# Optimization experiments

Hardware: AMD Instinct MI355X
Metric: run time of the kernel (lower is better)

Reference implementation:

```python
import jax, jax.numpy as jnp
import numpy as np

EPS = 1e-7
B, F, C, H, W, D = 2, 2, 64, 32, 104, 96


def _pix_homog(h, w):
    ys, xs = jnp.meshgrid(jnp.arange(h, dtype=jnp.float32),
                          jnp.arange(w, dtype=jnp.float32), indexing='ij')
    return jnp.stack([xs.ravel(), ys.ravel(), jnp.ones(h * w, jnp.float32)], 0)  # [3, H*W]


def setup_inputs() -> dict:
    key = jax.random.key(0)
    k1, k2 = jax.random.split(key)
    current_feats = jax.random.normal(k1, (B, C, H, W), jnp.float32)
    lookup_feats = jax.random.normal(k2, (B, F, C, H, W), jnp.float32)

    rng = np.random.RandomState(0)
    # intrinsics at matching (feature) resolution, monodepth2-style
    Km = np.eye(4, dtype=np.float32)
    Km[0, 0] = 0.58 * W
    Km[1, 1] = 1.92 * H
    Km[0, 2] = 0.5 * W
    Km[1, 2] = 0.5 * H
    K = np.tile(Km[None], (B, 1, 1))
    invK = np.linalg.inv(K).astype(np.float32)

    # near-identity relative poses (small rotation perturbation + small translation)
    poses = np.tile(np.eye(4, dtype=np.float32)[None, None], (B, F, 1, 1))
    poses[:, :, :3, :3] += 0.02 * rng.randn(B, F, 3, 3).astype(np.float32)
    poses[:, :, :3, 3] = 0.1 * rng.randn(B, F, 3).astype(np.float32)

    depth_bins = jnp.linspace(0.1, 20.0, D, dtype=jnp.float32)
    return {
        'current_feats': current_feats,
        'lookup_feats': lookup_feats,
        'poses': jnp.asarray(poses),
        'K': jnp.asarray(K),
        'invK': jnp.asarray(invK),
        'depth_bins': depth_bins,
    }


def _grid_sample_zeros(lfT, gx, gy, h, w):
    """Bilinear grid_sample, align_corners=True, padding_mode='zeros'.
    lfT: [B,F,H,W,C]; gx,gy: [B,F,D,H,W] in pixel coords. -> [B,F,D,H,W,C]"""
    x0 = jnp.floor(gx)
    y0 = jnp.floor(gy)
    x0i = x0.astype(jnp.int32)
    y0i = y0.astype(jnp.int32)
    wx1 = gx - x0
    wy1 = gy - y0
    wx0 = 1.0 - wx1
    wy0 = 1.0 - wy1
    bb = jnp.arange(lfT.shape[0])[:, None, None, None, None]
    ff = jnp.arange(lfT.shape[1])[None, :, None, None, None]

    def corner(yi, xi, wgt):
        m = ((xi >= 0) & (xi < w) & (yi >= 0) & (yi < h)).astype(lfT.dtype)
        xc = jnp.clip(xi, 0, w - 1)
        yc = jnp.clip(yi, 0, h - 1)
        v = lfT[bb, ff, yc, xc]                      # [B,F,D,H,W,C]
        return v * (m * wgt)[..., None]

    return (corner(y0i, x0i, wy0 * wx0) + corner(y0i, x0i + 1, wy0 * wx1)
            + corner(y0i + 1, x0i, wy1 * wx0) + corner(y0i + 1, x0i + 1, wy1 * wx1))


def reference(current_feats, lookup_feats, poses, K, invK, depth_bins):
    b, c, h, w = current_feats.shape
    f = lookup_feats.shape[1]
    d = depth_bins.shape[0]

    # Backproject: world points for each hypothesised depth plane
    pix = _pix_homog(h, w)                                   # [3, HW]
    cam = jnp.einsum('bij,jn->bin', invK[:, :3, :3], pix)    # [B,3,HW]
    pts = depth_bins[None, :, None, None] * cam[:, None]     # [B,D,3,HW]
    world = jnp.concatenate([pts, jnp.ones((b, d, 1, h * w), pts.dtype)], 2)  # [B,D,4,HW]

    # Project into each lookup frame
    P = jnp.einsum('bij,bfjk->bfik', K, poses)[:, :, :3, :]  # [B,F,3,4]
    cpts = jnp.einsum('bfij,bdjn->bfdin', P, world)          # [B,F,D,3,HW]
    xy = cpts[:, :, :, :2] / (cpts[:, :, :, 2:3] + EPS)      # pixel coords [B,F,D,2,HW]
    xy = xy.reshape(b, f, d, 2, h, w)
    gx, gy = xy[:, :, :, 0], xy[:, :, :, 1]                  # [B,F,D,H,W]

    # edge mask (detach in original -> stop_gradient)
    sx, sy = jax.lax.stop_gradient(gx), jax.lax.stop_gradient(gy)
    edge = ((sx >= 2.0) & (sx <= w - 2) & (sy >= 2.0) & (sy <= h - 2)).astype(jnp.float32)
    interior = jnp.zeros((h, w), jnp.float32).at[2:-2, 2:-2].set(1.0)
    edge_mask = edge * interior                               # [B,F,D,H,W]

    # warp lookup features and L1-diff against current features
    lfT = lookup_feats.transpose(0, 1, 3, 4, 2)               # [B,F,H,W,C]
    warped = _grid_sample_zeros(lfT, gx, gy, h, w)            # [B,F,D,H,W,C]
    cur = current_feats.transpose(0, 2, 3, 1)                 # [B,H,W,C]
    diffs = jnp.abs(warped - cur[:, None, None]).mean(-1) * edge_mask  # [B,F,D,H,W]

    # skip lookup frames whose pose is all-zero
    valid = (poses.sum((-2, -1)) != 0).astype(jnp.float32)    # [B,F]
    diffs = diffs * valid[:, :, None, None, None]

    cost = diffs.sum(1)                                        # [B,D,H,W]
    counts = (diffs > 0).astype(jnp.float32).sum(1)
    cost = cost / (counts + EPS)

    # set missing values to per-pixel max over depth bins
    missing = (cost == 0.0)
    cmax = cost.max(1, keepdims=True)
    cost = jnp.where(missing, cmax, cost)
    return cost
```

## Files before the change

kernel.cpp:

```cpp
#include <hip/hip_runtime.h>
#include <math.h>

constexpr int B_ = 2, F_ = 2, C_ = 64, H_ = 32, W_ = 104, D_ = 96;
constexpr int HW_ = H_ * W_;
#define EPSF 1e-7f

constexpr size_t LFT_OFF  = 0;
constexpr size_t CURT_OFF = LFT_OFF + (size_t)B_ * F_ * HW_ * C_;

constexpr int NT_BLKS = (HW_ / 32) * (C_ / 32) * (B_ * F_ + B_);
constexpr int PXB   = 4;
constexpr int XT_   = W_ / PXB;
constexpr int DPAD  = D_ + 1;
constexpr int DPADI = D_ + 4;

template<int CTRL>
__device__ __forceinline__ float dpp_add(float x) {
    int y = __builtin_amdgcn_update_dpp(0, __float_as_int(x), CTRL, 0xf, 0xf, true);
    return x + __int_as_float(y);
}
__device__ __forceinline__ float group16_sum(float s) {
    s = dpp_add<0xB1>(s);
    s = dpp_add<0x4E>(s);
    s = dpp_add<0x141>(s);
    s = dpp_add<0x140>(s);
    return s;
}

__global__ __launch_bounds__(256) void prep_kernel(
        const float* __restrict__ cur, const float* __restrict__ lf,
        float* __restrict__ ws) {
    __shared__ float tile[32][33];
    int bid = blockIdx.x;
    int slice = bid / 208;
    int rem   = bid % 208;
    int nb = rem % 104, cb = rem / 104;
    const float* inS;
    float* outS;
    if (slice < B_ * F_) {
        inS  = lf + (size_t)slice * C_ * HW_;
        outS = ws + LFT_OFF + (size_t)slice * HW_ * C_;
    } else {
        int s2 = slice - B_ * F_;
        inS  = cur + (size_t)s2 * C_ * HW_;
        outS = ws + CURT_OFF + (size_t)s2 * HW_ * C_;
    }
    int t = threadIdx.x;
    int tx = t & 31, ty = t >> 5;
    int n0 = nb * 32, c0 = cb * 32;
    #pragma unroll
    for (int k = 0; k < 32; k += 8)
        tile[ty + k][tx] = inS[(size_t)(c0 + ty + k) * HW_ + n0 + tx];
    __syncthreads();
    #pragma unroll
    for (int k = 0; k < 32; k += 8)
        outS[(size_t)(n0 + ty + k) * C_ + c0 + tx] = tile[tx][ty + k];
}

__global__ __launch_bounds__(256, 6) void mega_kernel(
        const float* __restrict__ poses, const float* __restrict__ K,
        const float* __restrict__ invK, const float* __restrict__ depth_bins,
        const float* __restrict__ ws, float* __restrict__ out) {
    int t   = threadIdx.x;
    int bid = blockIdx.x;
    int xt  = bid % XT_;  int r = bid / XT_;
    int y   = r % H_;
    int b   = r / H_;

    if (y < 2 || y >= H_ - 2) {
        for (int k = t; k < PXB * D_; k += 256) {
            int d = k >> 2, px = k & 3;
            out[((size_t)(b * D_ + d) * H_ + y) * W_ + xt * PXB + px] = 0.0f;
        }
        return;
    }

    __shared__ int    offsL[F_][PXB][DPADI];
    __shared__ float4 wtsL [F_][PXB][DPAD];
    __shared__ float  costb[PXB][DPAD];
    __shared__ float  pmax[32][PXB];
    __shared__ float  cmaxb[PXB];

    {
        int pxA = t & 3;
        int xA  = xt * PXB + pxA;
        const float* iK = invK + (size_t)b * 16;
        float xf = (float)xA, yf = (float)y;
        float cam0 = __fmul_rn(iK[0], xf); cam0 = __fmaf_rn(iK[1], yf, cam0); cam0 = __fmaf_rn(iK[2],  1.0f, cam0);
        float cam1 = __fmul_rn(iK[4], xf); cam1 = __fmaf_rn(iK[5], yf, cam1); cam1 = __fmaf_rn(iK[6],  1.0f, cam1);
        float cam2 = __fmul_rn(iK[8], xf); cam2 = __fmaf_rn(iK[9], yf, cam2); cam2 = __fmaf_rn(iK[10], 1.0f, cam2);
        bool interior = (xA >= 2) && (xA <= W_ - 3);

        #pragma unroll
        for (int f = 0; f < F_; ++f) {
            const float* Kb   = K + (size_t)b * 16;
            const float* pose = poses + (size_t)(b * F_ + f) * 16;
            float P[12];
            #pragma unroll
            for (int i = 0; i < 3; ++i) {
                #pragma unroll
                for (int k = 0; k < 4; ++k) {
                    float acc = __fmul_rn(Kb[i*4+0], pose[0*4+k]);
                    acc = __fmaf_rn(Kb[i*4+1], pose[1*4+k], acc);
                    acc = __fmaf_rn(Kb[i*4+2], pose[2*4+k], acc);
                    acc = __fmaf_rn(Kb[i*4+3], pose[3*4+k], acc);
                    P[i*4+k] = acc;
                }
            }
            float vs = 0.f;
            #pragma unroll
            for (int j = 0; j < 16; ++j) vs += pose[j];
            bool valid = (vs != 0.f);

            #pragma unroll
            for (int k = 0; k < 2; ++k) {
                int idx = t + 256 * k;
                if (idx < PXB * D_) {
                    int dd = idx >> 2;
                    float depth = depth_bins[dd];
                    float p0 = __fmul_rn(depth, cam0);
                    float p1 = __fmul_rn(depth, cam1);
                    float p2 = __fmul_rn(depth, cam2);
                    float c0 = __fmul_rn(P[0], p0); c0 = __fmaf_rn(P[1], p1, c0); c0 = __fmaf_rn(P[2],  p2, c0); c0 = __fmaf_rn(P[3],  1.0f, c0);
                    float c1 = __fmul_rn(P[4], p0); c1 = __fmaf_rn(P[5], p1, c1); c1 = __fmaf_rn(P[6],  p2, c1); c1 = __fmaf_rn(P[7],  1.0f, c1);
                    float c2 = __fmul_rn(P[8], p0); c2 = __fmaf_rn(P[9], p1, c2); c2 = __fmaf_rn(P[10], p2, c2); c2 = __fmaf_rn(P[11], 1.0f, c2);
                    float denom = __fadd_rn(c2, EPSF);
                    float gx = c0 / denom;
                    float gy = c1 / denom;
                    bool m = valid && interior && (gx >= 2.0f) && (gx <= (float)(W_ - 2))
                                               && (gy >= 2.0f) && (gy <= (float)(H_ - 2));
                    if (m) {
                        float x0f = floorf(gx), y0f = floorf(gy);
                        int   x0  = (int)x0f,   y0  = (int)y0f;
                        float wx1 = gx - x0f, wy1 = gy - y0f;
                        float wx0 = 1.f - wx1, wy0 = 1.f - wy1;
                        wtsL[f][pxA][dd] = make_float4(wy0 * wx0, wy0 * wx1,
                                                       wy1 * wx0, wy1 * wx1);
                        offsL[f][pxA][dd] = (y0 * W_ + x0) * C_;
                    } else {
                        offsL[f][pxA][dd] = -1;
                        wtsL[f][pxA][dd] = make_float4(0.f, 0.f, 0.f, 0.f);
                    }
                }
            }
        }
    }
    __syncthreads();

    {
        int lane = t & 15, px = (t >> 4) & 3, half = t >> 6;
        int x = xt * PXB + px;
        const float4 cv = *(const float4*)(ws + CURT_OFF
                            + ((size_t)((b * H_ + y) * W_ + x)) * C_ + lane * 4);
        const float* lf0a = ws + LFT_OFF + (size_t)(b * F_ + 0) * HW_ * C_ + lane * 4;
        const float* lf0b = lf0a + W_ * C_;
        const float* lf1a = ws + LFT_OFF + (size_t)(b * F_ + 1) * HW_ * C_ + lane * 4;
        const float* lf1b = lf1a + W_ * C_;

        float4 cc0[4], cc1[4];
        int oprev0 = -1, oprev1 = -1;
        #pragma unroll
        for (int k = 0; k < 4; ++k)
            cc0[k] = cc1[k] = make_float4(0.f, 0.f, 0.f, 0.f);

        int dbeg = half * (D_ / 4);
        #pragma unroll 4
        for (int ki = 0; ki < D_ / 4; ++ki) {
            int dc = dbeg + ki;
            int    oc0 = offsL[0][px][dc], oc1 = offsL[1][px][dc];
            float4 wc0 = wtsL[0][px][dc],  wc1 = wtsL[1][px][dc];

            float costsum = 0.f, counts = 0.f;
            {
                bool m = (oc0 >= 0);
                if (m && oc0 != oprev0) {
                    cc0[0] = *(const float4*)(lf0a + oc0);
                    cc0[1] = *(const float4*)(lf0a + oc0 + C_);
                    cc0[2] = *(const float4*)(lf0b + oc0);
                    cc0[3] = *(const float4*)(lf0b + oc0 + C_);
                    oprev0 = oc0;
                }
                float s;
                s  = fabsf(cc0[0].x*wc0.x + cc0[1].x*wc0.y + cc0[2].x*wc0.z + cc0[3].x*wc0.w - cv.x);
                s += fabsf(cc0[0].y*wc0.x + cc0[1].y*wc0.y + cc0[2].y*wc0.z + cc0[3].y*wc0.w - cv.y);
                s += fabsf(cc0[0].z*wc0.x + cc0[1].z*wc0.y + cc0[2].z*wc0.z + cc0[3].z*wc0.w - cv.z);
                s += fabsf(cc0[0].w*wc0.x + cc0[1].w*wc0.y + cc0[2].w*wc0.z + cc0[3].w*wc0.w - cv.w);
                s = group16_sum(s);
                float diff = __fmul_rn(s, 1.0f / 64.0f) * (m ? 1.0f : 0.0f);
                costsum += diff;
                counts  += (diff > 0.f) ? 1.0f : 0.0f;
            }
            {
                bool m = (oc1 >= 0);
                if (m && oc1 != oprev1) {
                    cc1[0] = *(const float4*)(lf1a + oc1);
                    cc1[1] = *(const float4*)(lf1a + oc1 + C_);
                    cc1[2] = *(const float4*)(lf1b + oc1);
                    cc1[3] = *(const float4*)(lf1b + oc1 + C_);
                    oprev1 = oc1;
                }
                float s;
                s  = fabsf(cc1[0].x*wc1.x + cc1[1].x*wc1.y + cc1[2].x*wc1.z + cc1[3].x*wc1.w - cv.x);
                s += fabsf(cc1[0].y*wc1.x + cc1[1].y*wc1.y + cc1[2].y*wc1.z + cc1[3].y*wc1.w - cv.y);
                s += fabsf(cc1[0].z*wc1.x + cc1[1].z*wc1.y + cc1[2].z*wc1.z + cc1[3].z*wc1.w - cv.z);
                s += fabsf(cc1[0].w*wc1.x + cc1[1].w*wc1.y + cc1[2].w*wc1.z + cc1[3].w*wc1.w - cv.w);
                s = group16_sum(s);
                float diff = __fmul_rn(s, 1.0f / 64.0f) * (m ? 1.0f : 0.0f);
                costsum += diff;
                counts  += (diff > 0.f) ? 1.0f : 0.0f;
            }
            float cost = costsum * __builtin_amdgcn_rcpf(__fadd_rn(counts, EPSF));
            if (lane == 0) costb[px][dc] = cost;
        }
    }
    __syncthreads();

    {
        int j = t >> 2, px = t & 3;
        float v[3];
        if (t < 128) {
            float pm = 0.f;
            #pragma unroll
            for (int k = 0; k < 3; ++k) {
                v[k] = costb[px][j + 32 * k];
                pm = fmaxf(pm, v[k]);
            }
            pmax[j][px] = pm;
        }
        __syncthreads();
        if (t < PXB) {
            float cm = 0.f;
            #pragma unroll
            for (int jj = 0; jj < 32; ++jj) cm = fmaxf(cm, pmax[jj][t]);
            cmaxb[t] = cm;
        }
        __syncthreads();
        if (t < 128) {
            float cm = cmaxb[px];
            int x = xt * PXB + px;
            #pragma unroll
            for (int k = 0; k < 3; ++k) {
                int d = j + 32 * k;
                out[((size_t)(b * D_ + d) * H_ + y) * W_ + x] = (v[k] == 0.0f) ? cm : v[k];
            }
        }
    }
}

extern "C" void kernel_launch(void* const* d_in, const int* in_sizes, int n_in,
                              void* d_out, int out_size, void* d_ws, size_t ws_size,
                              hipStream_t stream) {
    const float* cur        = (const float*)d_in[0];
    const float* lf         = (const float*)d_in[1];
    const float* poses      = (const float*)d_in[2];
    const float* K          = (const float*)d_in[3];
    const float* invK       = (const float*)d_in[4];
    const float* depth_bins = (const float*)d_in[5];
    float* out = (float*)d_out;
    float* ws  = (float*)d_ws;

    prep_kernel<<<NT_BLKS, 256, 0, stream>>>(cur, lf, ws);
    mega_kernel<<<B_ * H_ * XT_, 256, 0, stream>>>(poses, K, invK, depth_bins, ws, out);
}
```

Baseline: 96.09 us.

## Store transposed lookup features as bf16 and vectorize offset loads

The prep kernel now writes the transposed lookup features in bf16 (round-to-nearest-even) instead of fp32, halving the gather bytes the main kernel reads per bilinear corner. The main kernel unpacks bf16 pairs to float, reads four depth offsets at once with int4 shared loads, and rewrites the interpolation as explicit FMA chains. The reduced precision of the lookup features may change numerics against the fp32 reference beyond tolerance.

```diff
diff --git a/kernel.cpp b/kernel.cpp
--- a/kernel.cpp
+++ b/kernel.cpp
@@ -5,8 +5,8 @@
 constexpr int HW_ = H_ * W_;
 #define EPSF 1e-7f
 
-constexpr size_t LFT_OFF  = 0;
-constexpr size_t CURT_OFF = LFT_OFF + (size_t)B_ * F_ * HW_ * C_;
+constexpr size_t LFT_ELEMS  = (size_t)B_ * F_ * HW_ * C_;
+constexpr size_t CURT_OFF_F = LFT_ELEMS / 2;
 
 constexpr int NT_BLKS = (HW_ / 32) * (C_ / 32) * (B_ * F_ + B_);
 constexpr int PXB   = 4;
@@ -25,6 +25,18 @@
     s = dpp_add<0x141>(s);
     s = dpp_add<0x140>(s);
     return s;
+}
+
+__device__ __forceinline__ ushort f2bf(float f) {
+    unsigned u = __float_as_uint(f);
+    u += 0x7FFFu + ((u >> 16) & 1u);
+    return (ushort)(u >> 16);
+}
+__device__ __forceinline__ float4 bf4(uint2 q) {
+    return make_float4(__uint_as_float(q.x << 16),
+                       __uint_as_float(q.x & 0xffff0000u),
+                       __uint_as_float(q.y << 16),
+                       __uint_as_float(q.y & 0xffff0000u));
 }
 
 __global__ __launch_bounds__(256) void prep_kernel(
@@ -35,16 +47,9 @@
     int slice = bid / 208;
     int rem   = bid % 208;
     int nb = rem % 104, cb = rem / 104;
-    const float* inS;
-    float* outS;
-    if (slice < B_ * F_) {
-        inS  = lf + (size_t)slice * C_ * HW_;
-        outS = ws + LFT_OFF + (size_t)slice * HW_ * C_;
-    } else {
-        int s2 = slice - B_ * F_;
-        inS  = cur + (size_t)s2 * C_ * HW_;
-        outS = ws + CURT_OFF + (size_t)s2 * HW_ * C_;
-    }
+    const float* inS = (slice < B_ * F_)
+        ? lf  + (size_t)slice * C_ * HW_
+        : cur + (size_t)(slice - B_ * F_) * C_ * HW_;
     int t = threadIdx.x;
     int tx = t & 31, ty = t >> 5;
     int n0 = nb * 32, c0 = cb * 32;
@@ -52,9 +57,17 @@
     for (int k = 0; k < 32; k += 8)
         tile[ty + k][tx] = inS[(size_t)(c0 + ty + k) * HW_ + n0 + tx];
     __syncthreads();
-    #pragma unroll
-    for (int k = 0; k < 32; k += 8)
-        outS[(size_t)(n0 + ty + k) * C_ + c0 + tx] = tile[tx][ty + k];
+    if (slice < B_ * F_) {
+        ushort* outS = (ushort*)ws + (size_t)slice * HW_ * C_;
+        #pragma unroll
+        for (int k = 0; k < 32; k += 8)
+            outS[(size_t)(n0 + ty + k) * C_ + c0 + tx] = f2bf(tile[tx][ty + k]);
+    } else {
+        float* outS = ws + CURT_OFF_F + (size_t)(slice - B_ * F_) * HW_ * C_;
+        #pragma unroll
+        for (int k = 0; k < 32; k += 8)
+            outS[(size_t)(n0 + ty + k) * C_ + c0 + tx] = tile[tx][ty + k];
+    }
 }
 
 __global__ __launch_bounds__(256, 6) void mega_kernel(
@@ -75,7 +88,7 @@
         return;
     }
 
-    __shared__ int    offsL[F_][PXB][DPADI];
+    __shared__ alignas(16) int offsL[F_][PXB][DPADI];
     __shared__ float4 wtsL [F_][PXB][DPAD];
     __shared__ float  costb[PXB][DPAD];
     __shared__ float  pmax[32][PXB];
@@ -150,12 +163,13 @@
     {
         int lane = t & 15, px = (t >> 4) & 3, half = t >> 6;
         int x = xt * PXB + px;
-        const float4 cv = *(const float4*)(ws + CURT_OFF
+        const float4 cv = *(const float4*)(ws + CURT_OFF_F
                             + ((size_t)((b * H_ + y) * W_ + x)) * C_ + lane * 4);
-        const float* lf0a = ws + LFT_OFF + (size_t)(b * F_ + 0) * HW_ * C_ + lane * 4;
-        const float* lf0b = lf0a + W_ * C_;
-        const float* lf1a = ws + LFT_OFF + (size_t)(b * F_ + 1) * HW_ * C_ + lane * 4;
-        const float* lf1b = lf1a + W_ * C_;
+        const ushort* lfbase = (const ushort*)ws;
+        const ushort* lf0a = lfbase + (size_t)(b * F_ + 0) * HW_ * C_ + lane * 4;
+        const ushort* lf0b = lf0a + W_ * C_;
+        const ushort* lf1a = lfbase + (size_t)(b * F_ + 1) * HW_ * C_ + lane * 4;
+        const ushort* lf1b = lf1a + W_ * C_;
 
         float4 cc0[4], cc1[4];
         int oprev0 = -1, oprev1 = -1;
@@ -164,53 +178,63 @@
             cc0[k] = cc1[k] = make_float4(0.f, 0.f, 0.f, 0.f);
 
         int dbeg = half * (D_ / 4);
-        #pragma unroll 4
-        for (int ki = 0; ki < D_ / 4; ++ki) {
-            int dc = dbeg + ki;
-            int    oc0 = offsL[0][px][dc], oc1 = offsL[1][px][dc];
-            float4 wc0 = wtsL[0][px][dc],  wc1 = wtsL[1][px][dc];
-
-            float costsum = 0.f, counts = 0.f;
-            {
-                bool m = (oc0 >= 0);
-                if (m && oc0 != oprev0) {
-                    cc0[0] = *(const float4*)(lf0a + oc0);
-                    cc0[1] = *(const float4*)(lf0a + oc0 + C_);
-                    cc0[2] = *(const float4*)(lf0b + oc0);
-                    cc0[3] = *(const float4*)(lf0b + oc0 + C_);
-                    oprev0 = oc0;
-                }
-                float s;
-                s  = fabsf(cc0[0].x*wc0.x + cc0[1].x*wc0.y + cc0[2].x*wc0.z + cc0[3].x*wc0.w - cv.x);
-                s += fabsf(cc0[0].y*wc0.x + cc0[1].y*wc0.y + cc0[2].y*wc0.z + cc0[3].y*wc0.w - cv.y);
-                s += fabsf(cc0[0].z*wc0.x + cc0[1].z*wc0.y + cc0[2].z*wc0.z + cc0[3].z*wc0.w - cv.z);
-                s += fabsf(cc0[0].w*wc0.x + cc0[1].w*wc0.y + cc0[2].w*wc0.z + cc0[3].w*wc0.w - cv.w);
-                s = group16_sum(s);
-                float diff = __fmul_rn(s, 1.0f / 64.0f) * (m ? 1.0f : 0.0f);
-                costsum += diff;
-                counts  += (diff > 0.f) ? 1.0f : 0.0f;
-            }
-            {
-                bool m = (oc1 >= 0);
-                if (m && oc1 != oprev1) {
-                    cc1[0] = *(const float4*)(lf1a + oc1);
-                    cc1[1] = *(const float4*)(lf1a + oc1 + C_);
-                    cc1[2] = *(const float4*)(lf1b + oc1);
-                    cc1[3] = *(const float4*)(lf1b + oc1 + C_);
-                    oprev1 = oc1;
-                }
-                float s;
-                s  = fabsf(cc1[0].x*wc1.x + cc1[1].x*wc1.y + cc1[2].x*wc1.z + cc1[3].x*wc1.w - cv.x);
-                s += fabsf(cc1[0].y*wc1.x + cc1[1].y*wc1.y + cc1[2].y*wc1.z + cc1[3].y*wc1.w - cv.y);
-                s += fabsf(cc1[0].z*wc1.x + cc1[1].z*wc1.y + cc1[2].z*wc1.z + cc1[3].z*wc1.w - cv.z);
-                s += fabsf(cc1[0].w*wc1.x + cc1[1].w*wc1.y + cc1[2].w*wc1.z + cc1[3].w*wc1.w - cv.w);
-                s = group16_sum(s);
-                float diff = __fmul_rn(s, 1.0f / 64.0f) * (m ? 1.0f : 0.0f);
-                costsum += diff;
-                counts  += (diff > 0.f) ? 1.0f : 0.0f;
-            }
-            float cost = costsum * __builtin_amdgcn_rcpf(__fadd_rn(counts, EPSF));
-            if (lane == 0) costb[px][dc] = cost;
+        for (int ki4 = 0; ki4 < D_ / 16; ++ki4) {
+            int dc4 = dbeg + ki4 * 4;
+            int4 oq0 = *(const int4*)&offsL[0][px][dc4];
+            int4 oq1 = *(const int4*)&offsL[1][px][dc4];
+            int oa0[4] = {oq0.x, oq0.y, oq0.z, oq0.w};
+            int oa1[4] = {oq1.x, oq1.y, oq1.z, oq1.w};
+
+            #pragma unroll
+            for (int j = 0; j < 4; ++j) {
+                int dc = dc4 + j;
+                int    oc0 = oa0[j],          oc1 = oa1[j];
+                float4 wc0 = wtsL[0][px][dc], wc1 = wtsL[1][px][dc];
+
+                float costsum = 0.f, counts = 0.f;
+                {
+                    bool m = (oc0 >= 0);
+                    if (m && oc0 != oprev0) {
+                        uint2 q0 = *(const uint2*)(lf0a + oc0);
+                        uint2 q1 = *(const uint2*)(lf0a + oc0 + C_);
+                        uint2 q2 = *(const uint2*)(lf0b + oc0);
+                        uint2 q3 = *(const uint2*)(lf0b + oc0 + C_);
+                        cc0[0] = bf4(q0); cc0[1] = bf4(q1); cc0[2] = bf4(q2); cc0[3] = bf4(q3);
+                        oprev0 = oc0;
+                    }
+                    float a0 = __fmaf_rn(cc0[0].x, wc0.x, __fmaf_rn(cc0[1].x, wc0.y, __fmaf_rn(cc0[2].x, wc0.z, __fmaf_rn(cc0[3].x, wc0.w, -cv.x))));
+                    float a1 = __fmaf_rn(cc0[0].y, wc0.x, __fmaf_rn(cc0[1].y, wc0.y, __fmaf_rn(cc0[2].y, wc0.z, __fmaf_rn(cc0[3].y, wc0.w, -cv.y))));
+                    float a2 = __fmaf_rn(cc0[0].z, wc0.x, __fmaf_rn(cc0[1].z, wc0.y, __fmaf_rn(cc0[2].z, wc0.z, __fmaf_rn(cc0[3].z, wc0.w, -cv.z))));
+                    float a3 = __fmaf_rn(cc0[0].w, wc0.x, __fmaf_rn(cc0[1].w, wc0.y, __fmaf_rn(cc0[2].w, wc0.z, __fmaf_rn(cc0[3].w, wc0.w, -cv.w))));
+                    float s = (fabsf(a0) + fabsf(a1)) + (fabsf(a2) + fabsf(a3));
+                    s = group16_sum(s);
+                    float diff = __fmul_rn(s, 1.0f / 64.0f) * (m ? 1.0f : 0.0f);
+                    costsum += diff;
+                    counts  += (diff > 0.f) ? 1.0f : 0.0f;
+                }
+                {
+                    bool m = (oc1 >= 0);
+                    if (m && oc1 != oprev1) {
+                        uint2 q0 = *(const uint2*)(lf1a + oc1);
+                        uint2 q1 = *(const uint2*)(lf1a + oc1 + C_);
+                        uint2 q2 = *(const uint2*)(lf1b + oc1);
+                        uint2 q3 = *(const uint2*)(lf1b + oc1 + C_);
+                        cc1[0] = bf4(q0); cc1[1] = bf4(q1); cc1[2] = bf4(q2); cc1[3] = bf4(q3);
+                        oprev1 = oc1;
+                    }
+                    float a0 = __fmaf_rn(cc1[0].x, wc1.x, __fmaf_rn(cc1[1].x, wc1.y, __fmaf_rn(cc1[2].x, wc1.z, __fmaf_rn(cc1[3].x, wc1.w, -cv.x))));
+                    float a1 = __fmaf_rn(cc1[0].y, wc1.x, __fmaf_rn(cc1[1].y, wc1.y, __fmaf_rn(cc1[2].y, wc1.z, __fmaf_rn(cc1[3].y, wc1.w, -cv.y))));
+                    float a2 = __fmaf_rn(cc1[0].z, wc1.x, __fmaf_rn(cc1[1].z, wc1.y, __fmaf_rn(cc1[2].z, wc1.z, __fmaf_rn(cc1[3].z, wc1.w, -cv.z))));
+                    float a3 = __fmaf_rn(cc1[0].w, wc1.x, __fmaf_rn(cc1[1].w, wc1.y, __fmaf_rn(cc1[2].w, wc1.z, __fmaf_rn(cc1[3].w, wc1.w, -cv.w))));
+                    float s = (fabsf(a0) + fabsf(a1)) + (fabsf(a2) + fabsf(a3));
+                    s = group16_sum(s);
+                    float diff = __fmul_rn(s, 1.0f / 64.0f) * (m ? 1.0f : 0.0f);
+                    costsum += diff;
+                    counts  += (diff > 0.f) ? 1.0f : 0.0f;
+                }
+                float cost = costsum * __builtin_amdgcn_rcpf(__fadd_rn(counts, EPSF));
+                if (lane == 0) costb[px][dc] = cost;
+            }
         }
     }
     __syncthreads();
```

After: 103.2 us. 1.07x slower.
